# Kernel optimization log

Hardware: AMD Instinct MI355X
Metric: run time of the kernel (lower is better)

The kernel has to match this reference:

```python
import jax, jax.numpy as jnp
import numpy as np

N, E = 131072, 64
REL_SIZES = {0: (262144, 1), 1: (524288, 2), 2: (393216, 3)}  # idx_len, arity


def _mish(x):
    return x * jnp.tanh(jax.nn.softplus(x))


def _mlp(x, rw, rb, ow, ob):
    # torch MLP: output(input + mish(residual(input)))
    return (x + _mish(x @ rw + rb)) @ ow + ob


def setup_inputs() -> dict:
    key = jax.random.key(0)
    ks = jax.random.split(key, 16)

    def lin(k, fi, fo):
        k1, k2 = jax.random.split(k)
        lim = 1.0 / np.sqrt(fi)
        w = jax.random.uniform(k1, (fi, fo), jnp.float32, -lim, lim)
        b = jax.random.uniform(k2, (fo,), jnp.float32, -lim, lim)
        return w, b

    inp = {"obj_emb": jax.random.normal(ks[0], (N, E), jnp.float32)}
    for r in range(3):
        L, _ = REL_SIZES[r]
        inp[f"rel{r}_idx"] = jax.random.randint(ks[1 + r], (L,), 0, N, jnp.int64)
    for r in range(3):
        _, a = REL_SIZES[r]
        d = a * E
        w, b = lin(ks[4 + 2 * r], d, d)
        inp[f"r{r}_res_w"], inp[f"r{r}_res_b"] = w, b
        w, b = lin(ks[5 + 2 * r], d, d)
        inp[f"r{r}_out_w"], inp[f"r{r}_out_b"] = w, b
    w, b = lin(ks[10], 2 * E, 2 * E)
    inp["upd_res_w"], inp["upd_res_b"] = w, b
    w, b = lin(ks[11], 2 * E, E)
    inp["upd_out_w"], inp["upd_out_b"] = w, b
    return inp


def _forward(obj_emb, idxs, rel_params, upd_params):
    n, e = obj_emb.shape
    outs = []
    for (idx, a), (rw, rb, ow, ob) in zip(idxs, rel_params):
        g = obj_emb[idx].reshape(-1, a * e)          # gather -> [T, a*E]
        outs.append((idx, _mlp(g, rw, rb, ow, ob).reshape(-1, e)))
    # First scatter_reduce_('amax', include_self=False): positions written by
    # relation 0 ignore the initial 0; all other positions keep/compete with 0.
    written0 = jnp.zeros((n,), bool).at[idxs[0][0]].set(True)
    m = jnp.broadcast_to(jnp.where(written0[:, None], -jnp.inf, 0.0).astype(obj_emb.dtype), (n, e))
    for idx, out in outs:
        m = m.at[idx].max(out)
    m = jax.lax.stop_gradient(m)
    s = jnp.full((n, e), 1e-16, obj_emb.dtype)
    for idx, out in outs:
        s = s.at[idx].add(jnp.exp(12.0 * (out - m[idx])))
    max_msg = jnp.log(s) / 12.0 + m
    return _mlp(jnp.concatenate([max_msg, obj_emb], axis=1), *upd_params)


def reference(obj_emb, rel0_idx, rel1_idx, rel2_idx,
              r0_res_w, r0_res_b, r0_out_w, r0_out_b,
              r1_res_w, r1_res_b, r1_out_w, r1_out_b,
              r2_res_w, r2_res_b, r2_out_w, r2_out_b,
              upd_res_w, upd_res_b, upd_out_w, upd_out_b):
    idxs = [(rel0_idx, 1), (rel1_idx, 2), (rel2_idx, 3)]
    rel_params = [
        (r0_res_w, r0_res_b, r0_out_w, r0_out_b),
        (r1_res_w, r1_res_b, r1_out_w, r1_out_b),
        (r2_res_w, r2_res_b, r2_out_w, r2_out_b),
    ]
    return _forward(obj_emb, idxs, rel_params,
                    (upd_res_w, upd_res_b, upd_out_w, upd_out_b))
```

## Files before the change

### kernel.cpp

```cpp
#include <hip/hip_runtime.h>
#include <stdint.h>

typedef unsigned short u16;
typedef __bf16 bf16x8 __attribute__((ext_vector_type(8)));
typedef float floatx4 __attribute__((ext_vector_type(4)));

#define N_OBJ    131072
#define L0R      262144
#define L1R      524288
#define L2R      393216
#define TOTI     (L0R + L1R + L2R)


__device__ __forceinline__ float bf2f(u16 u) {
  union { uint32_t i; float f; } v; v.i = ((uint32_t)u) << 16; return v.f;
}
__device__ __forceinline__ u16 f2bf(float f) {
  union { float f; uint32_t i; } v; v.f = f;
  uint32_t r = (v.i + 0x7FFFu + ((v.i >> 16) & 1u)) >> 16;
  return (u16)r;
}
__device__ __forceinline__ uint4 pack8(const float* sp) {
  float4 f0 = *(const float4*)(sp);
  float4 f1 = *(const float4*)(sp + 4);
  uint4 v;
  v.x = (uint32_t)f2bf(f0.x) | ((uint32_t)f2bf(f0.y) << 16);
  v.y = (uint32_t)f2bf(f0.z) | ((uint32_t)f2bf(f0.w) << 16);
  v.z = (uint32_t)f2bf(f1.x) | ((uint32_t)f2bf(f1.y) << 16);
  v.w = (uint32_t)f2bf(f1.z) | ((uint32_t)f2bf(f1.w) << 16);
  return v;
}
__device__ __forceinline__ float mish_f(float x) {
  float t = __expf(fminf(x, 30.f));
  float u = 1.f + t; u = u * u;
  return x * (u - 1.f) / (u + 1.f);
}

__global__ __launch_bounds__(256) void ebf_kernel(
    const float* __restrict__ src, u16* __restrict__ dst)
{
  size_t g = (size_t)blockIdx.x * 256 + threadIdx.x;
  *(uint4*)(dst + g * 8) = pack8(src + g * 8);
}

__global__ __launch_bounds__(256) void norm_kernel(
    const int* __restrict__ r0, const int* __restrict__ r1,
    const int* __restrict__ r2, int* __restrict__ n, int* __restrict__ cnt,
    unsigned char* __restrict__ flag)
{
  int g = blockIdx.x * 256 + (int)threadIdx.x;
  const int* src; int off;
  if (g < L0R)              { src = r0; off = g; }
  else if (g < L0R + L1R)   { src = r1; off = g - L0R; }
  else                      { src = r2; off = g - L0R - L1R; }
  int lane = (int)threadIdx.x & 63;
  int probe = src[2 * lane + 1];
  bool i64 = (__ballot(probe == 0) == ~0ull);
  int v = i64 ? src[2 * off] : src[off];
  n[g] = v;
  if (g < L0R) flag[v] = 1;
  if (cnt) atomicAdd(&cnt[v], 1);
}

__global__ __launch_bounds__(256) void prep_kernel(
    const float* w0, const float* w1, const float* w2, const float* w3,
    const float* w4, const float* w5, const float* w6, const float* w7,
    u16* __restrict__ wt)
{
  int b = blockIdx.x;
  const float* srcs[8] = {w0, w1, w2, w3, w4, w5, w6, w7};
  const int fi[8]   = {64, 64, 128, 128, 192, 192, 128, 128};
  const int fo[8]   = {64, 64, 128, 128, 192, 192, 128, 64};
  const int boff[9] = {0, 16, 32, 96, 160, 304, 448, 512, 544};
  const int woff[8] = {0, 4096, 8192, 24576, 40960, 77824, 114688, 131072};
  int m = 0;
  #pragma unroll
  for (int j = 0; j < 8; ++j) if (b >= boff[j + 1]) m = j + 1;
  int e = (b - boff[m]) * 256 + (int)threadIdx.x;
  int k = e / fo[m];
  int n = e - k * fo[m];
  wt[woff[m] + n * fi[m] + k] = f2bf(srcs[m][e]);
}

__global__ __launch_bounds__(256) void scan_a(
    const int* __restrict__ count, int* __restrict__ thrpre,
    int* __restrict__ blocksum)
{
  int tid = (int)threadIdx.x, b = blockIdx.x;
  int o = b * 1024 + tid * 4;
  int t = count[o] + count[o + 1] + count[o + 2] + count[o + 3];
  __shared__ int sd[256];
  sd[tid] = t; __syncthreads();
  for (int off = 1; off < 256; off <<= 1) {
    int v = (tid >= off) ? sd[tid - off] : 0;
    __syncthreads();
    sd[tid] += v;
    __syncthreads();
  }
  thrpre[b * 256 + tid] = sd[tid] - t;
  if (tid == 255) blocksum[b] = sd[tid];
}
__global__ __launch_bounds__(128) void scan_b(int* __restrict__ blocksum)
{
  int tid = (int)threadIdx.x;
  int t = blocksum[tid];
  __shared__ int sd[128];
  sd[tid] = t; __syncthreads();
  for (int off = 1; off < 128; off <<= 1) {
    int v = (tid >= off) ? sd[tid - off] : 0;
    __syncthreads();
    sd[tid] += v;
    __syncthreads();
  }
  blocksum[tid] = sd[tid] - t;
}
__global__ __launch_bounds__(256) void scan_c(
    const int* __restrict__ count, const int* __restrict__ thrpre,
    const int* __restrict__ blocksum, int* __restrict__ offsets,
    int* __restrict__ cursor)
{
  int tid = (int)threadIdx.x, b = blockIdx.x;
  int o = b * 1024 + tid * 4;
  int base = blocksum[b] + thrpre[b * 256 + tid];
  #pragma unroll
  for (int j = 0; j < 4; ++j) {
    offsets[o + j] = base;
    cursor[o + j] = base;
    base += count[o + j];
  }
}

template<int D, int DOUT, int MODE, int EBF>
__global__ __launch_bounds__(256, (D >= 192) ? 3 : 4) void mlp_kernel(
    const float* __restrict__ srcF, const u16* __restrict__ srcB,
    const u16* __restrict__ srcM, const int* __restrict__ idx,
    const u16* __restrict__ rwt, const float* __restrict__ rb,
    const u16* __restrict__ owt, const float* __restrict__ ob,
    float* __restrict__ dstF, float* __restrict__ sAt,
    u16* __restrict__ msg, int* __restrict__ cursor)
{
  constexpr int A = D / 64;
  constexpr int PITCH = D + 8;
  constexpr int KI = D / 32;
  constexpr int CT1 = D / 64;
  constexpr int CT2 = DOUT / 64;
  __shared__ alignas(16) u16 g_lds[64 * PITCH];
  __shared__ float b1_lds[D];
  __shared__ float b2_lds[DOUT];
  __shared__ int i_lds[64 * A];
  __shared__ int p_lds[64 * A];

  const int tid = threadIdx.x;
  const int wave = tid >> 6;
  const int lane = tid & 63;
  const int q = lane >> 4;
  const int i = lane & 15;
  const int t0 = blockIdx.x * 64;

  for (int c = tid; c < D; c += 256) b1_lds[c] = rb[c];
  for (int c = tid; c < DOUT; c += 256) b2_lds[c] = ob[c];
  if (MODE != 1) {
    for (int c = tid; c < 64 * A; c += 256) {
      int obj = idx[t0 * A + c];
      i_lds[c] = obj;
      if (MODE == 0) p_lds[c] = atomicAdd(&cursor[obj], 1);
    }
  }

  for (int c = tid; c < 64 * A * 8; c += 256) {
    int e = c >> 3, p = c & 7;
    int r = e / A, sl = e - r * A;
    uint4 val;
    if (MODE != 1) {
      int obj = idx[(t0 + r) * A + sl];
      val = EBF ? *(const uint4*)(srcB + (size_t)obj * 64 + p * 8)
                : pack8(srcF + (size_t)obj * 64 + p * 8);
    } else {
      if (sl == 0) val = *(const uint4*)(srcM + (size_t)(t0 + r) * 64 + p * 8);
      else val = EBF ? *(const uint4*)(srcB + (size_t)(t0 + r) * 64 + p * 8)
                     : pack8(srcF + (size_t)(t0 + r) * 64 + p * 8);
    }
    *(uint4*)(&g_lds[r * PITCH + sl * 64 + p * 8]) = val;
  }
  __syncthreads();

  bf16x8 af[KI];

  bf16x8 b1[CT1][KI];
  #pragma unroll
  for (int j = 0; j < CT1; ++j)
    #pragma unroll
    for (int k = 0; k < KI; ++k)
      b1[j][k] = *(const bf16x8*)(rwt +
          (size_t)((wave * CT1 + j) * 16 + i) * D + k * 32 + q * 8);

  floatx4 acc1[4][CT1];
  #pragma unroll
  for (int rt = 0; rt < 4; ++rt)
    #pragma unroll
    for (int j = 0; j < CT1; ++j) acc1[rt][j] = (floatx4)0.f;

  #pragma unroll
  for (int rt = 0; rt < 4; ++rt) {
    #pragma unroll
    for (int k = 0; k < KI; ++k)
      af[k] = *(const bf16x8*)(&g_lds[(rt * 16 + i) * PITCH + k * 32 + q * 8]);
    #pragma unroll
    for (int j = 0; j < CT1; ++j)
      #pragma unroll
      for (int k = 0; k < KI; ++k)
        acc1[rt][j] = __builtin_amdgcn_mfma_f32_16x16x32_bf16(
            af[k], b1[j][k], acc1[rt][j], 0, 0, 0);
  }
  __syncthreads();

  #pragma unroll
  for (int rt = 0; rt < 4; ++rt)
    #pragma unroll
    for (int j = 0; j < CT1; ++j) {
      int col = (wave * CT1 + j) * 16 + i;
      #pragma unroll
      for (int r = 0; r < 4; ++r) {
        int row = rt * 16 + q * 4 + r;
        float h = acc1[rt][j][r] + b1_lds[col];
        float g = bf2f(g_lds[row * PITCH + col]);
        g_lds[row * PITCH + col] = f2bf(g + mish_f(h));
      }
    }
  __syncthreads();

  bf16x8 b2[CT2][KI];
  #pragma unroll
  for (int j = 0; j < CT2; ++j)
    #pragma unroll
    for (int k = 0; k < KI; ++k)
      b2[j][k] = *(const bf16x8*)(owt +
          (size_t)((wave * CT2 + j) * 16 + i) * D + k * 32 + q * 8);

  floatx4 acc2[4][CT2];
  #pragma unroll
  for (int rt = 0; rt < 4; ++rt)
    #pragma unroll
    for (int j = 0; j < CT2; ++j) acc2[rt][j] = (floatx4)0.f;

  #pragma unroll
  for (int rt = 0; rt < 4; ++rt) {
    #pragma unroll
    for (int k = 0; k < KI; ++k)
      af[k] = *(const bf16x8*)(&g_lds[(rt * 16 + i) * PITCH + k * 32 + q * 8]);
    #pragma unroll
    for (int j = 0; j < CT2; ++j)
      #pragma unroll
      for (int k = 0; k < KI; ++k)
        acc2[rt][j] = __builtin_amdgcn_mfma_f32_16x16x32_bf16(
            af[k], b2[j][k], acc2[rt][j], 0, 0, 0);
  }

  #pragma unroll
  for (int rt = 0; rt < 4; ++rt)
    #pragma unroll
    for (int j = 0; j < CT2; ++j) {
      int col = (wave * CT2 + j) * 16 + i;
      #pragma unroll
      for (int r = 0; r < 4; ++r) {
        int row = rt * 16 + q * 4 + r;
        float y = acc2[rt][j][r] + b2_lds[col];
        if (MODE == 0) {
          int slot = col >> 6, cc = col & 63;
          int pos = p_lds[row * A + slot];
          msg[(size_t)pos * 64 + cc] = f2bf(__expf(fminf(12.f * y, 82.f)));
        } else if (MODE == 2) {
          int slot = col >> 6, cc = col & 63;
          int obj = i_lds[row * A + slot];
          atomicAdd(&sAt[(size_t)obj * 64 + cc], __expf(fminf(12.f * y, 82.f)));
        } else {
          dstF[(size_t)(t0 + row) * 64 + col] = y;
        }
      }
    }
}

__global__ __launch_bounds__(256) void reduce_kernel(
    const u16* __restrict__ msg, const int* __restrict__ count,
    const int* __restrict__ offsets, const unsigned char* __restrict__ flag,
    u16* __restrict__ maxmsg)
{
  int wv = (int)threadIdx.x >> 6, lane = (int)threadIdx.x & 63;
  int o = blockIdx.x * 4 + wv;
  int deg = count[o], start = offsets[o];
  int rg = lane >> 3;
  int c8 = (lane & 7) * 8;
  const u16* base = msg + (size_t)start * 64 + c8;
  float s[8] = {0.f, 0.f, 0.f, 0.f, 0.f, 0.f, 0.f, 0.f};
  for (int row = rg; row < deg; row += 8) {
    union { uint4 v; u16 a[8]; } ld;
    ld.v = *(const uint4*)(base + (size_t)row * 64);
    #pragma unroll
    for (int k = 0; k < 8; ++k) s[k] += bf2f(ld.a[k]);
  }
  #pragma unroll
  for (int m = 8; m < 64; m <<= 1)
    #pragma unroll
    for (int k = 0; k < 8; ++k) s[k] += __shfl_xor(s[k], m);
  if (rg == 0) {
    float add = flag[o] ? 1e-37f : 1e-16f;
    u16 tmp[8];
    #pragma unroll
    for (int k = 0; k < 8; ++k)
      tmp[k] = f2bf(__logf(s[k] + add) * (1.f / 12.f));
    *(uint4*)(maxmsg + (size_t)o * 64 + c8) = *(uint4*)tmp;
  }
}

__global__ __launch_bounds__(256) void final_kernel(
    const float* __restrict__ s, const unsigned char* __restrict__ flag,
    u16* __restrict__ maxmsg)
{
  int tid = (int)threadIdx.x;
  int o = blockIdx.x * 64 + (tid >> 2);
  int c0 = (tid & 3) * 16;
  float add = flag[o] ? 1e-37f : 1e-16f;
  const float* sp = s + (size_t)o * 64 + c0;
  u16* mp = maxmsg + (size_t)o * 64 + c0;
  u16 tmp[16];
  #pragma unroll
  for (int j = 0; j < 16; ++j)
    tmp[j] = f2bf(__logf(sp[j] + add) * (1.f / 12.f));
  *(uint4*)(mp)     = *(uint4*)(tmp);
  *(uint4*)(mp + 8) = *(uint4*)(tmp + 8);
}

extern "C" void kernel_launch(void* const* d_in, const int* in_sizes, int n_in,
                              void* d_out, int out_size, void* d_ws, size_t ws_size,
                              hipStream_t stream)
{
  (void)in_sizes; (void)n_in; (void)out_size;
  const float* obj_emb = (const float*)d_in[0];
  const float* r0rb = (const float*)d_in[5];
  const float* r0ob = (const float*)d_in[7];
  const float* r1rb = (const float*)d_in[9];
  const float* r1ob = (const float*)d_in[11];
  const float* r2rb = (const float*)d_in[13];
  const float* r2ob = (const float*)d_in[15];
  const float* urb  = (const float*)d_in[17];
  const float* uob  = (const float*)d_in[19];
  float* out = (float*)d_out;
  char* ws = (char*)d_ws;

  const size_t NEED1 = 174605312ull;
  const size_t NEED2 = NEED1 + 16777216ull;

  if (ws_size >= NEED1) {
    u16* msg           = (u16*)(ws);
    u16* wt            = (u16*)(ws + 150994944ull);
    unsigned char* flg = (unsigned char*)(ws + 151273472ull);
    u16* maxmsg        = (u16*)(ws + 151404544ull);
    int* nidx          = (int*)(ws + 168181760ull);
    int* count         = (int*)(ws + 172900352ull);
    int* offsets       = (int*)(ws + 173424640ull);
    int* cursor        = (int*)(ws + 173948928ull);
    int* thrpre        = (int*)(ws + 174473216ull);
    int* blocksum      = (int*)(ws + 174604288ull);
    u16* ebf           = (u16*)(ws + 174605312ull);
    bool use_ebf = ws_size >= NEED2;

    hipMemsetAsync(count, 0, N_OBJ * 4, stream);
    hipMemsetAsync(flg, 0, N_OBJ, stream);

    if (use_ebf) ebf_kernel<<<4096, 256, 0, stream>>>(obj_emb, ebf);
    norm_kernel<<<TOTI / 256, 256, 0, stream>>>(
        (const int*)d_in[1], (const int*)d_in[2], (const int*)d_in[3],
        nidx, count, flg);
    prep_kernel<<<544, 256, 0, stream>>>(
        (const float*)d_in[4], (const float*)d_in[6], (const float*)d_in[8],
        (const float*)d_in[10], (const float*)d_in[12], (const float*)d_in[14],
        (const float*)d_in[16], (const float*)d_in[18], wt);
    scan_a<<<128, 256, 0, stream>>>(count, thrpre, blocksum);
    scan_b<<<1, 128, 0, stream>>>(blocksum);
    scan_c<<<128, 256, 0, stream>>>(count, thrpre, blocksum, offsets, cursor);

    if (use_ebf) {
      mlp_kernel<64, 64, 0, 1><<<4096, 256, 0, stream>>>(
          obj_emb, ebf, nullptr, nidx, wt + 0, r0rb, wt + 4096, r0ob,
          nullptr, nullptr, msg, cursor);
      mlp_kernel<128, 128, 0, 1><<<4096, 256, 0, stream>>>(
          obj_emb, ebf, nullptr, nidx + L0R, wt + 8192, r1rb, wt + 24576, r1ob,
          nullptr, nullptr, msg, cursor);
      mlp_kernel<192, 192, 0, 1><<<2048, 256, 0, stream>>>(
          obj_emb, ebf, nullptr, nidx + L0R + L1R, wt + 40960, r2rb, wt + 77824, r2ob,
          nullptr, nullptr, msg, cursor);
      reduce_kernel<<<N_OBJ / 4, 256, 0, stream>>>(msg, count, offsets, flg, maxmsg);
      mlp_kernel<128, 64, 1, 1><<<2048, 256, 0, stream>>>(
          obj_emb, ebf, maxmsg, nullptr, wt + 114688, urb, wt + 131072, uob,
          out, nullptr, nullptr, nullptr);
    } else {
      mlp_kernel<64, 64, 0, 0><<<4096, 256, 0, stream>>>(
          obj_emb, nullptr, nullptr, nidx, wt + 0, r0rb, wt + 4096, r0ob,
          nullptr, nullptr, msg, cursor);
      mlp_kernel<128, 128, 0, 0><<<4096, 256, 0, stream>>>(
          obj_emb, nullptr, nullptr, nidx + L0R, wt + 8192, r1rb, wt + 24576, r1ob,
          nullptr, nullptr, msg, cursor);
      mlp_kernel<192, 192, 0, 0><<<2048, 256, 0, stream>>>(
          obj_emb, nullptr, nullptr, nidx + L0R + L1R, wt + 40960, r2rb, wt + 77824, r2ob,
          nullptr, nullptr, msg, cursor);
      reduce_kernel<<<N_OBJ / 4, 256, 0, stream>>>(msg, count, offsets, flg, maxmsg);
      mlp_kernel<128, 64, 1, 0><<<2048, 256, 0, stream>>>(
          obj_emb, nullptr, maxmsg, nullptr, wt + 114688, urb, wt + 131072, uob,
          out, nullptr, nullptr, nullptr);
    }
  } else {
    float* s           = (float*)(ws);
    u16* wt            = (u16*)(ws + 33554432ull);
    unsigned char* flg = (unsigned char*)(ws + 33832960ull);
    u16* maxmsg        = (u16*)(ws + 33964032ull);
    int* nidx          = (int*)(ws + 50741248ull);

    hipMemsetAsync(s, 0, 64ull * N_OBJ * 4ull, stream);
    hipMemsetAsync(flg, 0, N_OBJ, stream);

    norm_kernel<<<TOTI / 256, 256, 0, stream>>>(
        (const int*)d_in[1], (const int*)d_in[2], (const int*)d_in[3],
        nidx, nullptr, flg);
    prep_kernel<<<544, 256, 0, stream>>>(
        (const float*)d_in[4], (const float*)d_in[6], (const float*)d_in[8],
        (const float*)d_in[10], (const float*)d_in[12], (const float*)d_in[14],
        (const float*)d_in[16], (const float*)d_in[18], wt);

    mlp_kernel<64, 64, 2, 0><<<4096, 256, 0, stream>>>(
        obj_emb, nullptr, nullptr, nidx, wt + 0, r0rb, wt + 4096, r0ob,
        nullptr, s, nullptr, nullptr);
    mlp_kernel<128, 128, 2, 0><<<4096, 256, 0, stream>>>(
        obj_emb, nullptr, nullptr, nidx + L0R, wt + 8192, r1rb, wt + 24576, r1ob,
        nullptr, s, nullptr, nullptr);
    mlp_kernel<192, 192, 2, 0><<<2048, 256, 0, stream>>>(
        obj_emb, nullptr, nullptr, nidx + L0R + L1R, wt + 40960, r2rb, wt + 77824, r2ob,
        nullptr, s, nullptr, nullptr);

    final_kernel<<<N_OBJ / 64, 256, 0, stream>>>(s, flg, maxmsg);

    mlp_kernel<128, 64, 1, 0><<<2048, 256, 0, stream>>>(
        obj_emb, nullptr, maxmsg, nullptr, wt + 114688, urb, wt + 131072, uob,
        out, nullptr, nullptr, nullptr);
  }
}
```

Baseline: 416.0 us.

## Merge relation MLP launches and fuse segment reduction into update MLP

The three per-relation MLP launches become one merged grid that branches on block index into templated bodies sharing dynamic shared memory. The separate reduce kernel is removed and the log-sum-exp reduction over each object's CSR segment is done inside the update MLP's gather stage. This removes launch gaps, tail effects between kernels and the maxmsg round trip through global memory. In exchange the merged kernel is capped at the 192-wide variant's occupancy, and the in-block reduction is done by one thread per 8 columns serially over the degree, which may cause imbalance.

```diff
diff --git a/kernel.cpp b/kernel.cpp
--- a/kernel.cpp
+++ b/kernel.cpp
@@ -130,14 +130,306 @@
   }
 }
 
-template<int D, int DOUT, int MODE, int EBF>
-__global__ __launch_bounds__(256, (D >= 192) ? 3 : 4) void mlp_kernel(
-    const float* __restrict__ srcF, const u16* __restrict__ srcB,
-    const u16* __restrict__ srcM, const int* __restrict__ idx,
+template<int D, int DOUT, int EBF>
+__device__ __forceinline__ void mlp_body(
+    char* smem, const float* __restrict__ srcF, const u16* __restrict__ srcB,
+    const int* __restrict__ idx, int bidx,
     const u16* __restrict__ rwt, const float* __restrict__ rb,
     const u16* __restrict__ owt, const float* __restrict__ ob,
-    float* __restrict__ dstF, float* __restrict__ sAt,
     u16* __restrict__ msg, int* __restrict__ cursor)
+{
+  constexpr int A = D / 64;
+  constexpr int PITCH = D + 8;
+  constexpr int KI = D / 32;
+  constexpr int CT1 = D / 64;
+  constexpr int CT2 = DOUT / 64;
+  u16*   g_lds  = (u16*)smem;
+  float* b1_lds = (float*)(smem + 64 * PITCH * 2);
+  float* b2_lds = b1_lds + D;
+  int*   i_lds  = (int*)(b2_lds + DOUT);
+  int*   p_lds  = i_lds + 64 * A;
+
+  const int tid = threadIdx.x;
+  const int wave = tid >> 6;
+  const int lane = tid & 63;
+  const int q = lane >> 4;
+  const int i = lane & 15;
+  const int t0 = bidx * 64;
+
+  for (int c = tid; c < D; c += 256) b1_lds[c] = rb[c];
+  for (int c = tid; c < DOUT; c += 256) b2_lds[c] = ob[c];
+  for (int c = tid; c < 64 * A; c += 256) {
+    int obj = idx[t0 * A + c];
+    i_lds[c] = obj;
+    p_lds[c] = atomicAdd(&cursor[obj], 1);
+  }
+
+  for (int c = tid; c < 64 * A * 8; c += 256) {
+    int e = c >> 3, p = c & 7;
+    int r = e / A, sl = e - r * A;
+    int obj = idx[(t0 + r) * A + sl];
+    uint4 val = EBF ? *(const uint4*)(srcB + (size_t)obj * 64 + p * 8)
+                    : pack8(srcF + (size_t)obj * 64 + p * 8);
+    *(uint4*)(&g_lds[r * PITCH + sl * 64 + p * 8]) = val;
+  }
+  __syncthreads();
+
+  bf16x8 af[KI];
+
+  bf16x8 b1[CT1][KI];
+  #pragma unroll
+  for (int j = 0; j < CT1; ++j)
+    #pragma unroll
+    for (int k = 0; k < KI; ++k)
+      b1[j][k] = *(const bf16x8*)(rwt +
+          (size_t)((wave * CT1 + j) * 16 + i) * D + k * 32 + q * 8);
+
+  floatx4 acc1[4][CT1];
+  #pragma unroll
+  for (int rt = 0; rt < 4; ++rt)
+    #pragma unroll
+    for (int j = 0; j < CT1; ++j) acc1[rt][j] = (floatx4)0.f;
+
+  #pragma unroll
+  for (int rt = 0; rt < 4; ++rt) {
+    #pragma unroll
+    for (int k = 0; k < KI; ++k)
+      af[k] = *(const bf16x8*)(&g_lds[(rt * 16 + i) * PITCH + k * 32 + q * 8]);
+    #pragma unroll
+    for (int j = 0; j < CT1; ++j)
+      #pragma unroll
+      for (int k = 0; k < KI; ++k)
+        acc1[rt][j] = __builtin_amdgcn_mfma_f32_16x16x32_bf16(
+            af[k], b1[j][k], acc1[rt][j], 0, 0, 0);
+  }
+  __syncthreads();
+
+  #pragma unroll
+  for (int rt = 0; rt < 4; ++rt)
+    #pragma unroll
+    for (int j = 0; j < CT1; ++j) {
+      int col = (wave * CT1 + j) * 16 + i;
+      #pragma unroll
+      for (int r = 0; r < 4; ++r) {
+        int row = rt * 16 + q * 4 + r;
+        float h = acc1[rt][j][r] + b1_lds[col];
+        float g = bf2f(g_lds[row * PITCH + col]);
+        g_lds[row * PITCH + col] = f2bf(g + mish_f(h));
+      }
+    }
+  __syncthreads();
+
+  bf16x8 b2[CT2][KI];
+  #pragma unroll
+  for (int j = 0; j < CT2; ++j)
+    #pragma unroll
+    for (int k = 0; k < KI; ++k)
+      b2[j][k] = *(const bf16x8*)(owt +
+          (size_t)((wave * CT2 + j) * 16 + i) * D + k * 32 + q * 8);
+
+  floatx4 acc2[4][CT2];
+  #pragma unroll
+  for (int rt = 0; rt < 4; ++rt)
+    #pragma unroll
+    for (int j = 0; j < CT2; ++j) acc2[rt][j] = (floatx4)0.f;
+
+  #pragma unroll
+  for (int rt = 0; rt < 4; ++rt) {
+    #pragma unroll
+    for (int k = 0; k < KI; ++k)
+      af[k] = *(const bf16x8*)(&g_lds[(rt * 16 + i) * PITCH + k * 32 + q * 8]);
+    #pragma unroll
+    for (int j = 0; j < CT2; ++j)
+      #pragma unroll
+      for (int k = 0; k < KI; ++k)
+        acc2[rt][j] = __builtin_amdgcn_mfma_f32_16x16x32_bf16(
+            af[k], b2[j][k], acc2[rt][j], 0, 0, 0);
+  }
+
+  #pragma unroll
+  for (int rt = 0; rt < 4; ++rt)
+    #pragma unroll
+    for (int j = 0; j < CT2; ++j) {
+      int col = (wave * CT2 + j) * 16 + i;
+      int slot = col >> 6, cc = col & 63;
+      #pragma unroll
+      for (int r = 0; r < 4; ++r) {
+        int row = rt * 16 + q * 4 + r;
+        float y = acc2[rt][j][r] + b2_lds[col];
+        int pos = p_lds[row * A + slot];
+        msg[(size_t)pos * 64 + cc] = f2bf(__expf(fminf(12.f * y, 82.f)));
+      }
+    }
+}
+
+template<int EBF>
+__global__ __launch_bounds__(256, 3) void rel_merged(
+    const float* __restrict__ srcF, const u16* __restrict__ ebf,
+    const int* __restrict__ nidx, const u16* __restrict__ wt,
+    const float* __restrict__ r0rb, const float* __restrict__ r0ob,
+    const float* __restrict__ r1rb, const float* __restrict__ r1ob,
+    const float* __restrict__ r2rb, const float* __restrict__ r2ob,
+    u16* __restrict__ msg, int* __restrict__ cursor)
+{
+  extern __shared__ char smem[];
+  int b = blockIdx.x;
+  if (b < 4096)
+    mlp_body<64, 64, EBF>(smem, srcF, ebf, nidx, b,
+                          wt + 0, r0rb, wt + 4096, r0ob, msg, cursor);
+  else if (b < 8192)
+    mlp_body<128, 128, EBF>(smem, srcF, ebf, nidx + L0R, b - 4096,
+                            wt + 8192, r1rb, wt + 24576, r1ob, msg, cursor);
+  else
+    mlp_body<192, 192, EBF>(smem, srcF, ebf, nidx + L0R + L1R, b - 8192,
+                            wt + 40960, r2rb, wt + 77824, r2ob, msg, cursor);
+}
+
+template<int EBF>
+__global__ __launch_bounds__(256, 4) void upd_fused(
+    const float* __restrict__ srcF, const u16* __restrict__ ebf,
+    const u16* __restrict__ msg, const int* __restrict__ count,
+    const int* __restrict__ offsets, const unsigned char* __restrict__ flag,
+    const u16* __restrict__ rwt, const float* __restrict__ rb,
+    const u16* __restrict__ owt, const float* __restrict__ ob,
+    float* __restrict__ dstF)
+{
+  constexpr int D = 128, DOUT = 64;
+  constexpr int PITCH = D + 8;
+  constexpr int KI = D / 32;
+  constexpr int CT1 = 2, CT2 = 1;
+  __shared__ alignas(16) u16 g_lds[64 * PITCH];
+  __shared__ float b1_lds[D];
+  __shared__ float b2_lds[DOUT];
+
+  const int tid = threadIdx.x;
+  const int wave = tid >> 6;
+  const int lane = tid & 63;
+  const int q = lane >> 4;
+  const int i = lane & 15;
+  const int t0 = blockIdx.x * 64;
+
+  for (int c = tid; c < D; c += 256) b1_lds[c] = rb[c];
+  for (int c = tid; c < DOUT; c += 256) b2_lds[c] = ob[c];
+
+  for (int c = tid; c < 64 * 2 * 8; c += 256) {
+    int e = c >> 3, p = c & 7;
+    int r = e >> 1, sl = e & 1;
+    int o = t0 + r;
+    if (sl == 0) {
+      int deg = count[o], st = offsets[o];
+      const u16* bp = msg + (size_t)st * 64 + p * 8;
+      float s[8] = {0.f, 0.f, 0.f, 0.f, 0.f, 0.f, 0.f, 0.f};
+      for (int j = 0; j < deg; ++j) {
+        union { uint4 v; u16 a[8]; } ld;
+        ld.v = *(const uint4*)(bp + (size_t)j * 64);
+        #pragma unroll
+        for (int k = 0; k < 8; ++k) s[k] += bf2f(ld.a[k]);
+      }
+      float add = flag[o] ? 1e-37f : 1e-16f;
+      u16 tmp[8];
+      #pragma unroll
+      for (int k = 0; k < 8; ++k)
+        tmp[k] = f2bf(__logf(s[k] + add) * (1.f / 12.f));
+      *(uint4*)(&g_lds[r * PITCH + p * 8]) = *(uint4*)tmp;
+    } else {
+      uint4 val = EBF ? *(const uint4*)(ebf + (size_t)o * 64 + p * 8)
+                      : pack8(srcF + (size_t)o * 64 + p * 8);
+      *(uint4*)(&g_lds[r * PITCH + 64 + p * 8]) = val;
+    }
+  }
+  __syncthreads();
+
+  bf16x8 af[KI];
+
+  bf16x8 b1[CT1][KI];
+  #pragma unroll
+  for (int j = 0; j < CT1; ++j)
+    #pragma unroll
+    for (int k = 0; k < KI; ++k)
+      b1[j][k] = *(const bf16x8*)(rwt +
+          (size_t)((wave * CT1 + j) * 16 + i) * D + k * 32 + q * 8);
+
+  floatx4 acc1[4][CT1];
+  #pragma unroll
+  for (int rt = 0; rt < 4; ++rt)
+    #pragma unroll
+    for (int j = 0; j < CT1; ++j) acc1[rt][j] = (floatx4)0.f;
+
+  #pragma unroll
+  for (int rt = 0; rt < 4; ++rt) {
+    #pragma unroll
+    for (int k = 0; k < KI; ++k)
+      af[k] = *(const bf16x8*)(&g_lds[(rt * 16 + i) * PITCH + k * 32 + q * 8]);
+    #pragma unroll
+    for (int j = 0; j < CT1; ++j)
+      #pragma unroll
+      for (int k = 0; k < KI; ++k)
+        acc1[rt][j] = __builtin_amdgcn_mfma_f32_16x16x32_bf16(
+            af[k], b1[j][k], acc1[rt][j], 0, 0, 0);
+  }
+  __syncthreads();
+
+  #pragma unroll
+  for (int rt = 0; rt < 4; ++rt)
+    #pragma unroll
+    for (int j = 0; j < CT1; ++j) {
+      int col = (wave * CT1 + j) * 16 + i;
+      #pragma unroll
+      for (int r = 0; r < 4; ++r) {
+        int row = rt * 16 + q * 4 + r;
+        float h = acc1[rt][j][r] + b1_lds[col];
+        float g = bf2f(g_lds[row * PITCH + col]);
+        g_lds[row * PITCH + col] = f2bf(g + mish_f(h));
+      }
+    }
+  __syncthreads();
+
+  bf16x8 b2[CT2][KI];
+  #pragma unroll
+  for (int j = 0; j < CT2; ++j)
+    #pragma unroll
+    for (int k = 0; k < KI; ++k)
+      b2[j][k] = *(const bf16x8*)(owt +
+          (size_t)((wave * CT2 + j) * 16 + i) * D + k * 32 + q * 8);
+
+  floatx4 acc2[4][CT2];
+  #pragma unroll
+  for (int rt = 0; rt < 4; ++rt)
+    #pragma unroll
+    for (int j = 0; j < CT2; ++j) acc2[rt][j] = (floatx4)0.f;
+
+  #pragma unroll
+  for (int rt = 0; rt < 4; ++rt) {
+    #pragma unroll
+    for (int k = 0; k < KI; ++k)
+      af[k] = *(const bf16x8*)(&g_lds[(rt * 16 + i) * PITCH + k * 32 + q * 8]);
+    #pragma unroll
+    for (int j = 0; j < CT2; ++j)
+      #pragma unroll
+      for (int k = 0; k < KI; ++k)
+        acc2[rt][j] = __builtin_amdgcn_mfma_f32_16x16x32_bf16(
+            af[k], b2[j][k], acc2[rt][j], 0, 0, 0);
+  }
+
+  #pragma unroll
+  for (int rt = 0; rt < 4; ++rt) {
+    int col = wave * 16 + i;
+    #pragma unroll
+    for (int r = 0; r < 4; ++r) {
+      int row = rt * 16 + q * 4 + r;
+      dstF[(size_t)(t0 + row) * 64 + col] = acc2[0][0][r * 0 + 0] * 0.f
+          + acc2[rt][0][r] + b2_lds[col];
+    }
+  }
+}
+
+template<int D, int DOUT, int MODE>
+__global__ __launch_bounds__(256, (D >= 192) ? 3 : 4) void mlp_fb(
+    const float* __restrict__ srcF, const u16* __restrict__ srcM,
+    const int* __restrict__ idx,
+    const u16* __restrict__ rwt, const float* __restrict__ rb,
+    const u16* __restrict__ owt, const float* __restrict__ ob,
+    float* __restrict__ dstF, float* __restrict__ sAt)
 {
   constexpr int A = D / 64;
   constexpr int PITCH = D + 8;
@@ -148,7 +440,6 @@
   __shared__ float b1_lds[D];
   __shared__ float b2_lds[DOUT];
   __shared__ int i_lds[64 * A];
-  __shared__ int p_lds[64 * A];
 
   const int tid = threadIdx.x;
   const int wave = tid >> 6;
@@ -159,13 +450,8 @@
 
   for (int c = tid; c < D; c += 256) b1_lds[c] = rb[c];
   for (int c = tid; c < DOUT; c += 256) b2_lds[c] = ob[c];
-  if (MODE != 1) {
-    for (int c = tid; c < 64 * A; c += 256) {
-      int obj = idx[t0 * A + c];
-      i_lds[c] = obj;
-      if (MODE == 0) p_lds[c] = atomicAdd(&cursor[obj], 1);
-    }
-  }
+  if (MODE != 1)
+    for (int c = tid; c < 64 * A; c += 256) i_lds[c] = idx[t0 * A + c];
 
   for (int c = tid; c < 64 * A * 8; c += 256) {
     int e = c >> 3, p = c & 7;
@@ -173,19 +459,16 @@
     uint4 val;
     if (MODE != 1) {
       int obj = idx[(t0 + r) * A + sl];
-      val = EBF ? *(const uint4*)(srcB + (size_t)obj * 64 + p * 8)
-                : pack8(srcF + (size_t)obj * 64 + p * 8);
+      val = pack8(srcF + (size_t)obj * 64 + p * 8);
     } else {
       if (sl == 0) val = *(const uint4*)(srcM + (size_t)(t0 + r) * 64 + p * 8);
-      else val = EBF ? *(const uint4*)(srcB + (size_t)(t0 + r) * 64 + p * 8)
-                     : pack8(srcF + (size_t)(t0 + r) * 64 + p * 8);
+      else         val = pack8(srcF + (size_t)(t0 + r) * 64 + p * 8);
     }
     *(uint4*)(&g_lds[r * PITCH + sl * 64 + p * 8]) = val;
   }
   __syncthreads();
 
   bf16x8 af[KI];
-
   bf16x8 b1[CT1][KI];
   #pragma unroll
   for (int j = 0; j < CT1; ++j)
@@ -193,13 +476,11 @@
     for (int k = 0; k < KI; ++k)
       b1[j][k] = *(const bf16x8*)(rwt +
           (size_t)((wave * CT1 + j) * 16 + i) * D + k * 32 + q * 8);
-
   floatx4 acc1[4][CT1];
   #pragma unroll
   for (int rt = 0; rt < 4; ++rt)
     #pragma unroll
     for (int j = 0; j < CT1; ++j) acc1[rt][j] = (floatx4)0.f;
-
   #pragma unroll
   for (int rt = 0; rt < 4; ++rt) {
     #pragma unroll
@@ -213,7 +494,6 @@
             af[k], b1[j][k], acc1[rt][j], 0, 0, 0);
   }
   __syncthreads();
-
   #pragma unroll
   for (int rt = 0; rt < 4; ++rt)
     #pragma unroll
@@ -228,7 +508,6 @@
       }
     }
   __syncthreads();
-
   bf16x8 b2[CT2][KI];
   #pragma unroll
   for (int j = 0; j < CT2; ++j)
@@ -236,13 +515,11 @@
     for (int k = 0; k < KI; ++k)
       b2[j][k] = *(const bf16x8*)(owt +
           (size_t)((wave * CT2 + j) * 16 + i) * D + k * 32 + q * 8);
-
   floatx4 acc2[4][CT2];
   #pragma unroll
   for (int rt = 0; rt < 4; ++rt)
     #pragma unroll
     for (int j = 0; j < CT2; ++j) acc2[rt][j] = (floatx4)0.f;
-
   #pragma unroll
   for (int rt = 0; rt < 4; ++rt) {
     #pragma unroll
@@ -255,7 +532,6 @@
         acc2[rt][j] = __builtin_amdgcn_mfma_f32_16x16x32_bf16(
             af[k], b2[j][k], acc2[rt][j], 0, 0, 0);
   }
-
   #pragma unroll
   for (int rt = 0; rt < 4; ++rt)
     #pragma unroll
@@ -265,11 +541,7 @@
       for (int r = 0; r < 4; ++r) {
         int row = rt * 16 + q * 4 + r;
         float y = acc2[rt][j][r] + b2_lds[col];
-        if (MODE == 0) {
-          int slot = col >> 6, cc = col & 63;
-          int pos = p_lds[row * A + slot];
-          msg[(size_t)pos * 64 + cc] = f2bf(__expf(fminf(12.f * y, 82.f)));
-        } else if (MODE == 2) {
+        if (MODE == 2) {
           int slot = col >> 6, cc = col & 63;
           int obj = i_lds[row * A + slot];
           atomicAdd(&sAt[(size_t)obj * 64 + cc], __expf(fminf(12.f * y, 82.f)));
@@ -278,38 +550,6 @@
         }
       }
     }
-}
-
-__global__ __launch_bounds__(256) void reduce_kernel(
-    const u16* __restrict__ msg, const int* __restrict__ count,
-    const int* __restrict__ offsets, const unsigned char* __restrict__ flag,
-    u16* __restrict__ maxmsg)
-{
-  int wv = (int)threadIdx.x >> 6, lane = (int)threadIdx.x & 63;
-  int o = blockIdx.x * 4 + wv;
-  int deg = count[o], start = offsets[o];
-  int rg = lane >> 3;
-  int c8 = (lane & 7) * 8;
-  const u16* base = msg + (size_t)start * 64 + c8;
-  float s[8] = {0.f, 0.f, 0.f, 0.f, 0.f, 0.f, 0.f, 0.f};
-  for (int row = rg; row < deg; row += 8) {
-    union { uint4 v; u16 a[8]; } ld;
-    ld.v = *(const uint4*)(base + (size_t)row * 64);
-    #pragma unroll
-    for (int k = 0; k < 8; ++k) s[k] += bf2f(ld.a[k]);
-  }
-  #pragma unroll
-  for (int m = 8; m < 64; m <<= 1)
-    #pragma unroll
-    for (int k = 0; k < 8; ++k) s[k] += __shfl_xor(s[k], m);
-  if (rg == 0) {
-    float add = flag[o] ? 1e-37f : 1e-16f;
-    u16 tmp[8];
-    #pragma unroll
-    for (int k = 0; k < 8; ++k)
-      tmp[k] = f2bf(__logf(s[k] + add) * (1.f / 12.f));
-    *(uint4*)(maxmsg + (size_t)o * 64 + c8) = *(uint4*)tmp;
-  }
 }
 
 __global__ __launch_bounds__(256) void final_kernel(
@@ -354,7 +594,6 @@
     u16* msg           = (u16*)(ws);
     u16* wt            = (u16*)(ws + 150994944ull);
     unsigned char* flg = (unsigned char*)(ws + 151273472ull);
-    u16* maxmsg        = (u16*)(ws + 151404544ull);
     int* nidx          = (int*)(ws + 168181760ull);
     int* count         = (int*)(ws + 172900352ull);
     int* offsets       = (int*)(ws + 173424640ull);
@@ -380,33 +619,17 @@
     scan_c<<<128, 256, 0, stream>>>(count, thrpre, blocksum, offsets, cursor);
 
     if (use_ebf) {
-      mlp_kernel<64, 64, 0, 1><<<4096, 256, 0, stream>>>(
-          obj_emb, ebf, nullptr, nidx, wt + 0, r0rb, wt + 4096, r0ob,
-          nullptr, nullptr, msg, cursor);
-      mlp_kernel<128, 128, 0, 1><<<4096, 256, 0, stream>>>(
-          obj_emb, ebf, nullptr, nidx + L0R, wt + 8192, r1rb, wt + 24576, r1ob,
-          nullptr, nullptr, msg, cursor);
-      mlp_kernel<192, 192, 0, 1><<<2048, 256, 0, stream>>>(
-          obj_emb, ebf, nullptr, nidx + L0R + L1R, wt + 40960, r2rb, wt + 77824, r2ob,
-          nullptr, nullptr, msg, cursor);
-      reduce_kernel<<<N_OBJ / 4, 256, 0, stream>>>(msg, count, offsets, flg, maxmsg);
-      mlp_kernel<128, 64, 1, 1><<<2048, 256, 0, stream>>>(
-          obj_emb, ebf, maxmsg, nullptr, wt + 114688, urb, wt + 131072, uob,
-          out, nullptr, nullptr, nullptr);
+      rel_merged<1><<<10240, 256, 28672, stream>>>(
+          obj_emb, ebf, nidx, wt, r0rb, r0ob, r1rb, r1ob, r2rb, r2ob, msg, cursor);
+      upd_fused<1><<<2048, 256, 0, stream>>>(
+          obj_emb, ebf, msg, count, offsets, flg,
+          wt + 114688, urb, wt + 131072, uob, out);
     } else {
-      mlp_kernel<64, 64, 0, 0><<<4096, 256, 0, stream>>>(
-          obj_emb, nullptr, nullptr, nidx, wt + 0, r0rb, wt + 4096, r0ob,
-          nullptr, nullptr, msg, cursor);
-      mlp_kernel<128, 128, 0, 0><<<4096, 256, 0, stream>>>(
-          obj_emb, nullptr, nullptr, nidx + L0R, wt + 8192, r1rb, wt + 24576, r1ob,
-          nullptr, nullptr, msg, cursor);
-      mlp_kernel<192, 192, 0, 0><<<2048, 256, 0, stream>>>(
-          obj_emb, nullptr, nullptr, nidx + L0R + L1R, wt + 40960, r2rb, wt + 77824, r2ob,
-          nullptr, nullptr, msg, cursor);
-      reduce_kernel<<<N_OBJ / 4, 256, 0, stream>>>(msg, count, offsets, flg, maxmsg);
-      mlp_kernel<128, 64, 1, 0><<<2048, 256, 0, stream>>>(
-          obj_emb, nullptr, maxmsg, nullptr, wt + 114688, urb, wt + 131072, uob,
-          out, nullptr, nullptr, nullptr);
+      rel_merged<0><<<10240, 256, 28672, stream>>>(
+          obj_emb, ebf, nidx, wt, r0rb, r0ob, r1rb, r1ob, r2rb, r2ob, msg, cursor);
+      upd_fused<0><<<2048, 256, 0, stream>>>(
+          obj_emb, ebf, msg, count, offsets, flg,
+          wt + 114688, urb, wt + 131072, uob, out);
     }
   } else {
     float* s           = (float*)(ws);
@@ -426,20 +649,17 @@
         (const float*)d_in[10], (const float*)d_in[12], (const float*)d_in[14],
         (const float*)d_in[16], (const float*)d_in[18], wt);
 
-    mlp_kernel<64, 64, 2, 0><<<4096, 256, 0, stream>>>(
-        obj_emb, nullptr, nullptr, nidx, wt + 0, r0rb, wt + 4096, r0ob,
-        nullptr, s, nullptr, nullptr);
-    mlp_kernel<128, 128, 2, 0><<<4096, 256, 0, stream>>>(
-        obj_emb, nullptr, nullptr, nidx + L0R, wt + 8192, r1rb, wt + 24576, r1ob,
-        nullptr, s, nullptr, nullptr);
-    mlp_kernel<192, 192, 2, 0><<<2048, 256, 0, stream>>>(
-        obj_emb, nullptr, nullptr, nidx + L0R + L1R, wt + 40960, r2rb, wt + 77824, r2ob,
-        nullptr, s, nullptr, nullptr);
+    mlp_fb<64, 64, 2><<<4096, 256, 0, stream>>>(
+        obj_emb, nullptr, nidx, wt + 0, r0rb, wt + 4096, r0ob, nullptr, s);
+    mlp_fb<128, 128, 2><<<4096, 256, 0, stream>>>(
+        obj_emb, nullptr, nidx + L0R, wt + 8192, r1rb, wt + 24576, r1ob, nullptr, s);
+    mlp_fb<192, 192, 2><<<2048, 256, 0, stream>>>(
+        obj_emb, nullptr, nidx + L0R + L1R, wt + 40960, r2rb, wt + 77824, r2ob,
+        nullptr, s);
 
     final_kernel<<<N_OBJ / 64, 256, 0, stream>>>(s, flg, maxmsg);
 
-    mlp_kernel<128, 64, 1, 0><<<2048, 256, 0, stream>>>(
-        obj_emb, nullptr, maxmsg, nullptr, wt + 114688, urb, wt + 131072, uob,
-        out, nullptr, nullptr, nullptr);
-  }
-}
+    mlp_fb<128, 64, 1><<<2048, 256, 0, stream>>>(
+        obj_emb, maxmsg, nullptr, wt + 114688, urb, wt + 131072, uob, out, nullptr);
+  }
+}
```

Measured after the change: 399.9 us. -3.9%, faster.
